# Kernel optimization log

Hardware: AMD Instinct MI355X
Metric: run time of the kernel (lower is better)

The kernel has to match this reference:

```python
import jax, jax.numpy as jnp
import numpy as np

EMBED_DIM = 768
NUM_HEADS = 12
HEAD_DIM = EMBED_DIM // NUM_HEADS
KERNEL = 7


def _neighbor_index(size, kernel):
    # NATTEN border-clamped neighborhood: window start = clip(i - k//2, 0, size-k)
    start = np.clip(np.arange(size) - kernel // 2, 0, size - kernel)
    return jnp.asarray(start[:, None] + np.arange(kernel)[None, :])  # [size, kernel]


def setup_inputs() -> dict:
    key = jax.random.key(0)
    k1, k2, k3, k4, k5 = jax.random.split(key, 5)
    B, H, W, C = 8, 64, 64, EMBED_DIM
    x = jax.random.normal(k1, (B, H, W, C), dtype=jnp.float32)
    # torch.nn.Linear layout: weight [out, in]
    w_qkv = jax.random.normal(k2, (3 * C, C), dtype=jnp.float32) * (C ** -0.5)
    b_qkv = jax.random.normal(k3, (3 * C,), dtype=jnp.float32) * 0.02
    w_proj = jax.random.normal(k4, (C, C), dtype=jnp.float32) * (C ** -0.5)
    b_proj = jax.random.normal(k5, (C,), dtype=jnp.float32) * 0.02
    return {"x": x, "w_qkv": w_qkv, "b_qkv": b_qkv, "w_proj": w_proj, "b_proj": b_proj}


def reference(x, w_qkv, b_qkv, w_proj, b_proj):
    B, H, W, C = x.shape
    scale = HEAD_DIM ** -0.5
    qkv = (x @ w_qkv.T + b_qkv).reshape(B, H, W, 3, NUM_HEADS, HEAD_DIM)
    q = qkv[..., 0, :, :] * scale          # [B,H,W,nh,hd]
    k = qkv[..., 1, :, :]
    v = qkv[..., 2, :, :]

    idx_i = _neighbor_index(H, KERNEL)      # [H,K]
    idx_j = _neighbor_index(W, KERNEL)      # [W,K]

    # Logits over the K*K local neighborhood, one shifted gather per offset
    # (avoids materializing [B,H,W,K2,nh,hd]).
    logits = []
    for ki in range(KERNEL):
        k_row = jnp.take(k, idx_i[:, ki], axis=1)          # [B,H,W,nh,hd]
        for kj in range(KERNEL):
            k_nb = jnp.take(k_row, idx_j[:, kj], axis=2)   # [B,H,W,nh,hd]
            logits.append(jnp.einsum('bhwnd,bhwnd->bhwn', q, k_nb))
    logits = jnp.stack(logits, axis=-1)                     # [B,H,W,nh,K2]
    attn = jax.nn.softmax(logits, axis=-1)

    out = jnp.zeros((B, H, W, NUM_HEADS, HEAD_DIM), dtype=x.dtype)
    off = 0
    for ki in range(KERNEL):
        v_row = jnp.take(v, idx_i[:, ki], axis=1)
        for kj in range(KERNEL):
            v_nb = jnp.take(v_row, idx_j[:, kj], axis=2)
            out = out + attn[..., off][..., None] * v_nb
            off += 1

    out = out.reshape(B, H, W, C)
    return out @ w_proj.T + b_proj
```

## Files before the change

kernel.cpp:

```cpp
#include <hip/hip_runtime.h>
#include <cstddef>

#define EMBED   768
#define NHEADS  12
#define HDIM    64
#define KSZ     7
#define IMG_H   64
#define IMG_W   64
#define BATCH   8
#define NTOK    (BATCH*IMG_H*IMG_W)
#define QKV_N   (3*EMBED)

typedef __attribute__((ext_vector_type(8))) short  bf16x8;
typedef __attribute__((ext_vector_type(4))) float  f32x4;
typedef __attribute__((ext_vector_type(8))) unsigned short u16x8;
typedef __attribute__((ext_vector_type(4))) unsigned short u16x4;

__device__ __forceinline__ unsigned short f2bf(float f) {
    unsigned int u = __float_as_uint(f);
    u += 0x7FFFu + ((u >> 16) & 1u);
    return (unsigned short)(u >> 16);
}

__device__ __forceinline__ void gload_lds16(const void* g, void* l) {
    __builtin_amdgcn_global_load_lds(
        (const __attribute__((address_space(1))) unsigned int*)g,
        (__attribute__((address_space(3))) unsigned int*)l, 16, 0, 0);
}

__global__ __launch_bounds__(256)
void cvt_all_kernel(const float* __restrict__ x, const float* __restrict__ wq,
                    const float* __restrict__ wp, unsigned short* __restrict__ xbf,
                    unsigned short* __restrict__ wqbf, unsigned short* __restrict__ wpbf)
{
    const int NX = NTOK * EMBED / 4;
    const int NQ = QKV_N * EMBED / 4;
    const int NP = EMBED * EMBED / 4;
    int i = blockIdx.x * 256 + threadIdx.x;
    const float* src; unsigned short* dst; int j;
    if (i < NX)           { src = x;  dst = xbf;  j = i; }
    else if (i < NX + NQ) { src = wq; dst = wqbf; j = i - NX; }
    else if (i < NX + NQ + NP) { src = wp; dst = wpbf; j = i - NX - NQ; }
    else return;
    float4 f = *(const float4*)(src + (size_t)j * 4);
    u16x4 o;
    o[0] = f2bf(f.x); o[1] = f2bf(f.y); o[2] = f2bf(f.z); o[3] = f2bf(f.w);
    *(u16x4*)(dst + (size_t)j * 4) = o;
}

template<int BF16OUT>
__global__ __launch_bounds__(512)
void gemmT(const unsigned short* __restrict__ A, const unsigned short* __restrict__ W,
           const float* __restrict__ bias, void* __restrict__ outp,
           int M, int N, int K, int scaleN, float scale)
{
    __shared__ unsigned short lds[49152];
    const int t_ = threadIdx.x;
    const int l = t_ & 63, w = t_ >> 6;
    const int wm = w >> 1, wn = w & 1;

    const int nby = N >> 7;
    const int xcd = blockIdx.x & 7;
    const int loc = blockIdx.x >> 3;
    const int bmg = loc / nby;
    int bnq = loc - bmg * nby;
    if (bmg & 1) bnq = nby - 1 - bnq;
    const int bm = (xcd * ((M >> 8) >> 3) + bmg) << 8;
    const int bn = bnq << 7;

    const int kperm8 = ((l & 3) ^ ((l >> 3) & 3)) * 8;
    const unsigned short* gA = A + (size_t)(bm + 32 * w + (l >> 2)) * K + kperm8;
    const unsigned short* gB = W + (size_t)(bn + 16 * w + (l >> 2)) * K + kperm8;
    const size_t rstepA = (size_t)16 * K;

    const int foff = (l & 15) * 32 + (((l >> 4) ^ ((l >> 1) & 3)) * 8);
    const int aoff = wm * 4096;
    const int boff = 16384 + wn * 4096;

    f32x4 acc[4][4] = {};
    const int NT = K / 64;

#define BARRIER() asm volatile("s_barrier" ::: "memory")
#define WAITV3()  asm volatile("s_waitcnt vmcnt(3)" ::: "memory")
#define WAITV0()  asm volatile("s_waitcnt vmcnt(0)" ::: "memory")
#define STGA(c, k0, kk) do { \
        gload_lds16(gA + (size_t)(k0) + (kk) * 32,          lds + (c) + (4 * w + (kk)) * 512); \
        gload_lds16(gA + rstepA + (size_t)(k0) + (kk) * 32, lds + (c) + (4 * w + 2 + (kk)) * 512); } while (0)
#define STGB(c, k0, kk) \
        gload_lds16(gB + (size_t)(k0) + (kk) * 32, lds + (c) + 16384 + (2 * w + (kk)) * 512)

    STGA(0, 0, 0); STGB(0, 0, 0); STGA(0, 0, 1); STGB(0, 0, 1);
    WAITV3();
    BARRIER();

    for (int t = 0; t < NT; ++t) {
        const int c  = (t & 1) * 24576;
        const int cn = c ^ 24576;
        const int k1 = (t + 1) * 64;
        const bool pf = (t + 1) < NT;

        bf16x8 a[4], bq[4];

        #pragma unroll
        for (int m = 0; m < 4; ++m) a[m]  = *(const bf16x8*)(lds + c + aoff + (m * 2) * 512 + foff);
        #pragma unroll
        for (int n = 0; n < 4; ++n) bq[n] = *(const bf16x8*)(lds + c + boff + (n * 2) * 512 + foff);
        if (pf) { STGA(cn, k1, 0); STGB(cn, k1, 0); WAITV3(); }
        else    { WAITV0(); }
        BARRIER();
        __builtin_amdgcn_s_setprio(1);
        #pragma unroll
        for (int m = 0; m < 4; ++m)
            #pragma unroll
            for (int n = 0; n < 4; ++n)
                acc[m][n] = __builtin_amdgcn_mfma_f32_16x16x32_bf16(a[m], bq[n], acc[m][n], 0, 0, 0);
        __builtin_amdgcn_s_setprio(0);

        #pragma unroll
        for (int m = 0; m < 4; ++m) a[m]  = *(const bf16x8*)(lds + c + aoff + (m * 2 + 1) * 512 + foff);
        #pragma unroll
        for (int n = 0; n < 4; ++n) bq[n] = *(const bf16x8*)(lds + c + boff + (n * 2 + 1) * 512 + foff);
        if (pf) { STGA(cn, k1, 1); STGB(cn, k1, 1); WAITV3(); }
        BARRIER();
        __builtin_amdgcn_s_setprio(1);
        #pragma unroll
        for (int m = 0; m < 4; ++m)
            #pragma unroll
            for (int n = 0; n < 4; ++n)
                acc[m][n] = __builtin_amdgcn_mfma_f32_16x16x32_bf16(a[m], bq[n], acc[m][n], 0, 0, 0);
        __builtin_amdgcn_s_setprio(0);
    }
#undef BARRIER
#undef WAITV3
#undef WAITV0
#undef STGA
#undef STGB

    const int cr = (l >> 4) * 4;
    const int cc = l & 15;
    #pragma unroll
    for (int m = 0; m < 4; ++m) {
        #pragma unroll
        for (int n = 0; n < 4; ++n) {
            const int col = bn + wn * 64 + n * 16 + cc;
            const float bv = bias[col];
            const bool sc = col < scaleN;
            #pragma unroll
            for (int r = 0; r < 4; ++r) {
                const int row = bm + wm * 64 + m * 16 + cr + r;
                float v = acc[m][n][r] + bv;
                if (sc) v *= scale;
                if (BF16OUT) ((unsigned short*)outp)[(size_t)row * N + col] = f2bf(v);
                else         ((float*)outp)[(size_t)row * N + col] = v;
            }
        }
    }
}

__global__ __launch_bounds__(256)
void natten_kernel(const unsigned short* __restrict__ qkv, unsigned short* __restrict__ attn_bf)
{
    __shared__ unsigned short smem[4 * 5888];
    const int t = threadIdx.x;
    const int w = t >> 6, l = t & 63;
    const int c15 = l & 15, g = l >> 4;
    const int blk = blockIdx.x;
    const int tg = blk & 15;
    const int h = (blk >> 4) % NHEADS;
    const int b = blk / (16 * NHEADS);
    const int ti = (tg >> 2) * 16, tj = (tg & 3) * 16;
    const int pi0 = ti + w * 4;
    const int ws = min(max(pi0 - 3, 0), IMG_H - 10);
    const int cs = min(max(tj - 3, 0), IMG_W - 22);
    const int pixbase = b * 4096;

    unsigned short* Kl = smem + w * 5888;
    unsigned short* Vt = Kl + 2304;

    const int pj = tj + c15;
    const int sj = min(max(pj - 3, 0), IMG_W - KSZ);
    const unsigned int cm = 0x7Fu << (sj - cs);
    unsigned int rm[4];
    #pragma unroll
    for (int qt = 0; qt < 4; ++qt) {
        int si = min(max(pi0 + qt - 3, 0), IMG_H - KSZ);
        rm[qt] = 0x7Fu << (si - ws);
    }

    bf16x8 qf[4][2];
    #pragma unroll
    for (int qt = 0; qt < 4; ++qt)
        #pragma unroll
        for (int dh = 0; dh < 2; ++dh)
            qf[qt][dh] = *(const bf16x8*)(qkv +
                (size_t)(pixbase + (pi0 + qt) * 64 + tj + c15) * QKV_N + h * HDIM + dh * 32 + g * 8);

    const int sr = l & 31;
    const int h5 = l >> 5;
    const int sig = ((sr & 12) << 1) | ((sr & 16) >> 2) | (sr & 3);

    u16x8 kst[4], vst[4];

    {
        int ur = sr / 22, uc = sr - ur * 22;
        int prow = min(ws + ur, IMG_H - 1);
        const u16x8* gk = (const u16x8*)(qkv +
            (size_t)(pixbase + prow * 64 + cs + uc) * QKV_N + EMBED + h * HDIM + h5 * 32);
        #pragma unroll
        for (int i = 0; i < 4; ++i) { kst[i] = gk[i]; vst[i] = gk[i + 96]; }
    }
    #pragma unroll
    for (int i = 0; i < 4; ++i) *(u16x8*)(Kl + sr * 72 + h5 * 32 + i * 8) = kst[i];
    #pragma unroll
    for (int i = 0; i < 4; ++i)
        #pragma unroll
        for (int e = 0; e < 8; ++e)
            Vt[(h5 * 32 + i * 8 + e) * 56 + sig] = vst[i][e];

    f32x4 oacc[4][4] = {};
    float spart[4] = {0.f, 0.f, 0.f, 0.f};

    #pragma unroll 1
    for (int C = 0; C < 7; ++C) {
        if (C < 6) {
            int kk = (C + 1) * 32 + sr;
            int ur = kk / 22, uc = kk - ur * 22;
            int prow = min(ws + ur, IMG_H - 1);
            const u16x8* gk = (const u16x8*)(qkv +
                (size_t)(pixbase + prow * 64 + cs + uc) * QKV_N + EMBED + h * HDIM + h5 * 32);
            #pragma unroll
            for (int i = 0; i < 4; ++i) { kst[i] = gk[i]; vst[i] = gk[i + 96]; }
        }

        bf16x8 ka[2][2], vb[4];
        #pragma unroll
        for (int kt = 0; kt < 2; ++kt)
            #pragma unroll
            for (int dh = 0; dh < 2; ++dh)
                ka[kt][dh] = *(const bf16x8*)(Kl + (kt * 16 + c15) * 72 + dh * 32 + g * 8);
        #pragma unroll
        for (int dt = 0; dt < 4; ++dt)
            vb[dt] = *(const bf16x8*)(Vt + (dt * 16 + c15) * 56 + g * 8);

        int kk0 = C * 32 + 4 * g;
        int a22 = kk0 / 22;
        int uc0 = kk0 - a22 * 22;
        int urx[2][4]; unsigned int cb[2][4];
        #pragma unroll
        for (int kt = 0; kt < 2; ++kt)
            #pragma unroll
            for (int r = 0; r < 4; ++r) {
                int x = uc0 + kt * 16 + r;
                int wrp = x >= 22;
                int uc = x - (wrp ? 22 : 0);
                urx[kt][r] = a22 + wrp;
                cb[kt][r] = (cm >> uc) & 1u;
            }

        #pragma unroll
        for (int qt = 0; qt < 4; ++qt) {
            f32x4 s0 = {}, s1 = {};
            s0 = __builtin_amdgcn_mfma_f32_16x16x32_bf16(ka[0][0], qf[qt][0], s0, 0, 0, 0);
            s0 = __builtin_amdgcn_mfma_f32_16x16x32_bf16(ka[0][1], qf[qt][1], s0, 0, 0, 0);
            s1 = __builtin_amdgcn_mfma_f32_16x16x32_bf16(ka[1][0], qf[qt][0], s1, 0, 0, 0);
            s1 = __builtin_amdgcn_mfma_f32_16x16x32_bf16(ka[1][1], qf[qt][1], s1, 0, 0, 0);
            float p[2][4];
            #pragma unroll
            for (int r = 0; r < 4; ++r) {
                float e0 = exp2f(s0[r]);
                float e1 = exp2f(s1[r]);
                p[0][r] = ((rm[qt] >> urx[0][r]) & cb[0][r]) ? e0 : 0.f;
                p[1][r] = ((rm[qt] >> urx[1][r]) & cb[1][r]) ? e1 : 0.f;
                spart[qt] += p[0][r] + p[1][r];
            }
            unsigned int pk[4];
            asm("v_cvt_pk_bf16_f32 %0, %1, %2" : "=v"(pk[0]) : "v"(p[0][0]), "v"(p[0][1]));
            asm("v_cvt_pk_bf16_f32 %0, %1, %2" : "=v"(pk[1]) : "v"(p[0][2]), "v"(p[0][3]));
            asm("v_cvt_pk_bf16_f32 %0, %1, %2" : "=v"(pk[2]) : "v"(p[1][0]), "v"(p[1][1]));
            asm("v_cvt_pk_bf16_f32 %0, %1, %2" : "=v"(pk[3]) : "v"(p[1][2]), "v"(p[1][3]));
            bf16x8 pa = *(bf16x8*)pk;
            #pragma unroll
            for (int dt = 0; dt < 4; ++dt)
                oacc[qt][dt] = __builtin_amdgcn_mfma_f32_16x16x32_bf16(pa, vb[dt], oacc[qt][dt], 0, 0, 0);
        }

        if (C < 6) {
            #pragma unroll
            for (int i = 0; i < 4; ++i) *(u16x8*)(Kl + sr * 72 + h5 * 32 + i * 8) = kst[i];
            #pragma unroll
            for (int i = 0; i < 4; ++i)
                #pragma unroll
                for (int e = 0; e < 8; ++e)
                    Vt[(h5 * 32 + i * 8 + e) * 56 + sig] = vst[i][e];
        }
    }

    #pragma unroll
    for (int qt = 0; qt < 4; ++qt) {
        float s = spart[qt];
        s += __shfl_xor(s, 16);
        s += __shfl_xor(s, 32);
        #pragma unroll
        for (int r = 0; r < 4; ++r) {
            float sb = __shfl(s, 4 * g + r);
            float inv = __builtin_amdgcn_rcpf(sb);
            size_t obase = (size_t)(pixbase + (pi0 + qt) * 64 + tj + 4 * g + r) * EMBED
                         + h * HDIM + c15;
            #pragma unroll
            for (int dt = 0; dt < 4; ++dt)
                attn_bf[obase + dt * 16] = f2bf(oacc[qt][dt][r] * inv);
        }
    }
}

extern "C" void kernel_launch(void* const* d_in, const int* in_sizes, int n_in,
                              void* d_out, int out_size, void* d_ws, size_t ws_size,
                              hipStream_t stream)
{
    const float* x      = (const float*)d_in[0];
    const float* w_qkv  = (const float*)d_in[1];
    const float* b_qkv  = (const float*)d_in[2];
    const float* w_proj = (const float*)d_in[3];
    const float* b_proj = (const float*)d_in[4];
    float* out = (float*)d_out;

    char* p = (char*)d_ws;
    unsigned short* qkv = (unsigned short*)p;     p += (size_t)NTOK * QKV_N * 2;
    unsigned short* xbf = (unsigned short*)p;
    unsigned short* attn_bf = xbf;                p += (size_t)NTOK * EMBED * 2;
    unsigned short* wq_bf = (unsigned short*)p;   p += (size_t)QKV_N * EMBED * 2;
    unsigned short* wp_bf = (unsigned short*)p;

    const float scale = 0.125f * 1.44269504088896f;

    {
        const int ntot = (NTOK * EMBED + QKV_N * EMBED + EMBED * EMBED) / 4;
        cvt_all_kernel<<<(ntot + 255) / 256, 256, 0, stream>>>(
            x, w_qkv, w_proj, xbf, wq_bf, wp_bf);
    }

    {
        gemmT<1><<<(NTOK / 256) * (QKV_N / 128), 512, 0, stream>>>(
            xbf, wq_bf, b_qkv, qkv, NTOK, QKV_N, EMBED, EMBED, scale);
    }

    natten_kernel<<<BATCH * NHEADS * 16, 256, 0, stream>>>(qkv, attn_bf);

    {
        gemmT<0><<<(NTOK / 256) * (EMBED / 128), 512, 0, stream>>>(
            attn_bf, wp_bf, b_proj, out, NTOK, EMBED, EMBED, 0, 1.0f);
    }
}
```

Before: 331.6 us.

## Use 256x256 tile GEMM with 4-stage LDS pipeline for QKV projection

Adds a new GEMM kernel with 256x256 output tiles (8 waves as 2x4), a 4-deep LDS ring buffer fed by direct global-to-LDS loads, split MFMA phases with barriers and wave priority hints. It is used for the QKV projection in place of the 256x128 tile kernel. The larger tile raises arithmetic intensity and cuts A-matrix re-reads, at the cost of 128KB of LDS (one block per CU), more accumulator registers, and fewer blocks in the grid.

```diff
diff --git a/kernel.cpp b/kernel.cpp
--- a/kernel.cpp
+++ b/kernel.cpp
@@ -50,6 +50,111 @@
 
 template<int BF16OUT>
 __global__ __launch_bounds__(512)
+void gemm256(const unsigned short* __restrict__ A, const unsigned short* __restrict__ W,
+             const float* __restrict__ bias, void* __restrict__ outp,
+             int M, int N, int K, int scaleN, float scale)
+{
+    __shared__ unsigned short lds[65536];
+    const int t_ = threadIdx.x;
+    const int l = t_ & 63, w = t_ >> 6;
+    const int wm = w >> 2, wn = w & 3;
+
+    const int nby = N >> 8;
+    const int xcd = blockIdx.x & 7;
+    const int loc = blockIdx.x >> 3;
+    const int bmg = loc / nby;
+    int bnq = loc - bmg * nby;
+    if (bmg & 1) bnq = nby - 1 - bnq;
+    const int bm = (xcd * (((M >> 8) >> 3)) + bmg) << 8;
+    const int bn = bnq << 8;
+
+    const int kperm8 = ((l & 3) ^ ((l >> 3) & 3)) * 8;
+    const unsigned short* gA = A + (size_t)(bm + w * 16 + (l >> 2)) * K + kperm8;
+    const unsigned short* gB = W + (size_t)(bn + w * 16 + (l >> 2)) * K + kperm8;
+    const size_t rstep = (size_t)128 * K;
+
+    const int foff = (l & 15) * 32 + (((l >> 4) ^ ((l >> 1) & 3)) * 8);
+    const int aoff = wm * 8 * 512;
+    const int boff = 8192 + wn * 4 * 512;
+
+    f32x4 acc[8][4] = {};
+    const int NT = K / 32;
+
+#define BARRIER() asm volatile("s_barrier" ::: "memory")
+#define WAITV8()  asm volatile("s_waitcnt vmcnt(8)" ::: "memory")
+#define WAITV4()  asm volatile("s_waitcnt vmcnt(4)" ::: "memory")
+#define WAITV0()  asm volatile("s_waitcnt vmcnt(0)" ::: "memory")
+#define STG(tt) do { \
+        const int cc_ = ((tt) & 3) * 16384; const size_t ko_ = (size_t)(tt) * 32; \
+        gload_lds16(gA + ko_,         lds + cc_ + w * 512); \
+        gload_lds16(gA + rstep + ko_, lds + cc_ + (w + 8) * 512); \
+        gload_lds16(gB + ko_,         lds + cc_ + 8192 + w * 512); \
+        gload_lds16(gB + rstep + ko_, lds + cc_ + 8192 + (w + 8) * 512); } while (0)
+
+    STG(0); STG(1); STG(2);
+    WAITV8();
+    BARRIER();
+
+    for (int t = 0; t < NT; ++t) {
+        const int c = (t & 3) * 16384;
+        bf16x8 a[4], bq[4];
+
+        #pragma unroll
+        for (int m = 0; m < 4; ++m) a[m]  = *(const bf16x8*)(lds + c + aoff + m * 512 + foff);
+        #pragma unroll
+        for (int n = 0; n < 4; ++n) bq[n] = *(const bf16x8*)(lds + c + boff + n * 512 + foff);
+        BARRIER();
+        __builtin_amdgcn_s_setprio(1);
+        #pragma unroll
+        for (int m = 0; m < 4; ++m)
+            #pragma unroll
+            for (int n = 0; n < 4; ++n)
+                acc[m][n] = __builtin_amdgcn_mfma_f32_16x16x32_bf16(a[m], bq[n], acc[m][n], 0, 0, 0);
+        __builtin_amdgcn_s_setprio(0);
+
+        #pragma unroll
+        for (int m = 0; m < 4; ++m) a[m] = *(const bf16x8*)(lds + c + aoff + (4 + m) * 512 + foff);
+        if (t + 3 < NT)      { STG(t + 3); WAITV8(); }
+        else if (t == NT - 3)  WAITV4();
+        else if (t == NT - 2)  WAITV0();
+        BARRIER();
+        __builtin_amdgcn_s_setprio(1);
+        #pragma unroll
+        for (int m = 0; m < 4; ++m)
+            #pragma unroll
+            for (int n = 0; n < 4; ++n)
+                acc[4 + m][n] = __builtin_amdgcn_mfma_f32_16x16x32_bf16(a[m], bq[n], acc[4 + m][n], 0, 0, 0);
+        __builtin_amdgcn_s_setprio(0);
+    }
+#undef BARRIER
+#undef WAITV8
+#undef WAITV4
+#undef WAITV0
+#undef STG
+
+    const int cr = (l >> 4) * 4;
+    const int cc = l & 15;
+    #pragma unroll
+    for (int m = 0; m < 8; ++m) {
+        #pragma unroll
+        for (int n = 0; n < 4; ++n) {
+            const int col = bn + wn * 64 + n * 16 + cc;
+            const float bv = bias[col];
+            const bool sc = col < scaleN;
+            #pragma unroll
+            for (int r = 0; r < 4; ++r) {
+                const int row = bm + wm * 128 + m * 16 + cr + r;
+                float v = acc[m][n][r] + bv;
+                if (sc) v *= scale;
+                if (BF16OUT) ((unsigned short*)outp)[(size_t)row * N + col] = f2bf(v);
+                else         ((float*)outp)[(size_t)row * N + col] = v;
+            }
+        }
+    }
+}
+
+template<int BF16OUT>
+__global__ __launch_bounds__(512)
 void gemmT(const unsigned short* __restrict__ A, const unsigned short* __restrict__ W,
            const float* __restrict__ bias, void* __restrict__ outp,
            int M, int N, int K, int scaleN, float scale)
@@ -340,7 +445,7 @@
     }
 
     {
-        gemmT<1><<<(NTOK / 256) * (QKV_N / 128), 512, 0, stream>>>(
+        gemm256<1><<<(NTOK / 256) * (QKV_N / 256), 512, 0, stream>>>(
             xbf, wq_bf, b_qkv, qkv, NTOK, QKV_N, EMBED, EMBED, scale);
     }
 
```

New measurement: 315.4 us (median of 2 runs). 4.9% less time.
